# Kernel tuning notes

Measured on AMD Instinct MI355X. Metric: run time of the kernel, lower is better.

## Reference

```python
import jax, jax.numpy as jnp
import numpy as np

N_IN = 100000
N_OUT = 100000
K = 27        # kernel_volume = 3^3 for 3D hypercube kernel
M = 50000     # matched (in,out) pairs per kernel offset
C_IN = 128
C_OUT = 128


def setup_inputs() -> dict:
    key = jax.random.key(0)
    k1, k2, k3, k4, k5 = jax.random.split(key, 5)
    features = jax.random.normal(k1, (N_IN, C_IN), dtype=jnp.float32)
    kernel = jax.random.normal(k2, (K, C_IN, C_OUT), dtype=jnp.float32) * (1.0 / np.sqrt(C_IN * K))
    bias = jax.random.normal(k3, (1, C_OUT), dtype=jnp.float32) * 0.01
    in_map = jax.random.randint(k4, (K, M), 0, N_IN, dtype=jnp.int32)
    out_map = jax.random.randint(k5, (K, M), 0, N_OUT, dtype=jnp.int32)
    return {"features": features, "kernel": kernel, "bias": bias,
            "in_map": in_map, "out_map": out_map, "n_out": N_OUT}


def reference(features, kernel, bias, in_map, out_map, n_out):
    # Sparse convolution: per-offset gather -> GEMM -> scatter-add.
    gathered = features[in_map]                          # [K, M, C_in]
    prod = jnp.einsum('kmc,kcd->kmd', gathered, kernel)  # [K, M, C_out]
    out = jnp.zeros((n_out, kernel.shape[-1]), dtype=features.dtype)
    out = out.at[out_map.reshape(-1)].add(prod.reshape(-1, kernel.shape[-1]))
    out = out + bias                                     # bias broadcast [1, C_out]
    return out
```

## Files before the change

kernel.cpp:

```cpp
#include <hip/hip_runtime.h>
#include <hip/hip_bf16.h>

typedef __attribute__((ext_vector_type(4))) float  f32x4;
typedef __attribute__((ext_vector_type(8))) short  bf16x8;
typedef __attribute__((ext_vector_type(2))) float  float2v;
typedef __attribute__((ext_vector_type(4))) float  float4v;
typedef __attribute__((ext_vector_type(8))) unsigned short ushort8;
typedef __attribute__((ext_vector_type(2))) unsigned int uint2v;

#define CIO 128
#define BR  64
#define MAXT 96
#define NB_MAX 2048
#define CSPLIT 8
#define NPASS 6
#define STAGE_CAP 14336

__device__ __forceinline__ unsigned short f2bf(float f) {
  unsigned int u = __float_as_uint(f);
  u = u + 0x7fffu + ((u >> 16) & 1u);
  return (unsigned short)(u >> 16);
}
__device__ __forceinline__ float bf2f(unsigned short u) {
  return __uint_as_float(((unsigned int)u) << 16);
}

__device__ __forceinline__ void wgbar() {
  asm volatile("s_waitcnt lgkmcnt(0)" ::: "memory");
  __builtin_amdgcn_s_barrier();
  __builtin_amdgcn_sched_barrier(0);
}

__global__ void prep_wswz(const float* __restrict__ W,
                          unsigned short* __restrict__ Wswz, int total) {
  int i = blockIdx.x * 256 + threadIdx.x;
  if (i >= total) return;
  int lane = i & 63;
  int nf   = (i >> 6) & 7;
  int kb   = (i >> 9) & 3;
  int k    = i >> 11;
  int n    = nf * 16 + (lane & 15);
  int c0   = kb * 32 + (lane >> 4) * 8;
  ushort8 v;
  #pragma unroll
  for (int e = 0; e < 8; ++e)
    v[e] = f2bf(W[k * 16384 + (c0 + e) * 128 + n]);
  *(ushort8*)(Wswz + (size_t)i * 8) = v;
}

__global__ void prep_fbf(const float* __restrict__ f,
                         unsigned short* __restrict__ fbf, int total8) {
  int i = blockIdx.x * 256 + threadIdx.x;
  if (i >= total8) return;
  const float4v* s = (const float4v*)(f + (size_t)i * 8);
  float4v v0 = s[0], v1 = s[1];
  ushort8 o;
  o[0] = f2bf(v0.x); o[1] = f2bf(v0.y); o[2] = f2bf(v0.z); o[3] = f2bf(v0.w);
  o[4] = f2bf(v1.x); o[5] = f2bf(v1.y); o[6] = f2bf(v1.z); o[7] = f2bf(v1.w);
  *(ushort8*)(fbf + (size_t)i * 8) = o;
}

__global__ __launch_bounds__(1024) void count27p(const int* __restrict__ out_map,
                                                 int* __restrict__ counts,
                                                 int M, int NB, int nkey) {
  __shared__ int h[NB_MAX];
  int k = blockIdx.x, s = blockIdx.y, t = threadIdx.x;
  for (int i = t; i < NB; i += 1024) h[i] = 0;
  __syncthreads();
  int m0 = (int)(((long)s * M) / CSPLIT), m1 = (int)(((long)(s + 1) * M) / CSPLIT);
  for (int m = m0 + t; m < m1; m += 1024)
    atomicAdd(&h[out_map[k * M + m] / BR], 1);
  __syncthreads();
  for (int i = t; i < NB; i += 1024)
    counts[s * nkey + k * NB + i] = h[i];
}

__global__ __launch_bounds__(1024) void scan_p1(const int* __restrict__ counts,
                                                int* __restrict__ offs,
                                                int* __restrict__ bsum, int nkey) {
  __shared__ int part[1024];
  const int t = threadIdx.x;
  const int i = blockIdx.x * 1024 + t;
  int v = 0;
  if (i < nkey) {
    #pragma unroll
    for (int sl = 0; sl < CSPLIT; ++sl) v += counts[sl * nkey + i];
  }
  part[t] = v;
  __syncthreads();
  for (int d = 1; d < 1024; d <<= 1) {
    int x = (t >= d) ? part[t - d] : 0;
    __syncthreads();
    part[t] += x;
    __syncthreads();
  }
  if (i < nkey) offs[i] = part[t] - v;
  if (t == 1023) bsum[blockIdx.x] = part[1023];
}
__global__ void scan_p2(int* __restrict__ bsum, int nb) {
  if (threadIdx.x == 0) {
    int run = 0;
    for (int i = 0; i < nb; ++i) { int c = bsum[i]; bsum[i] = run; run += c; }
    bsum[nb] = run;
  }
}
__global__ __launch_bounds__(1024) void scan_p3(int* __restrict__ offs,
                                                const int* __restrict__ bsum,
                                                int nkey, int nb) {
  const int i = blockIdx.x * 1024 + threadIdx.x;
  if (i < nkey) offs[i] += bsum[blockIdx.x];
  if (i == 0) offs[nkey] = bsum[nb];
}

__global__ __launch_bounds__(1024) void scatter27c(const int* __restrict__ in_map,
                                                   const int* __restrict__ out_map,
                                                   const int* __restrict__ offs,
                                                   unsigned int* __restrict__ sorted,
                                                   int M, int NB) {
  __shared__ unsigned int stage[STAGE_CAP];
  __shared__ int pos[384];
  const int k = blockIdx.x, p = blockIdx.y, t = threadIdx.x;
  const int b0 = (int)(((long)p * NB) / NPASS);
  const int b1 = (int)(((long)(p + 1) * NB) / NPASS);
  const int nb = b1 - b0;
  const int sbase = offs[k * NB + b0];
  const int send  = offs[k * NB + b1];
  const int size  = send - sbase;
  for (int i = t; i < nb; i += 1024) pos[i] = offs[k * NB + b0 + i] - sbase;
  __syncthreads();
  if (size <= STAGE_CAP) {
    for (int m = t; m < M; m += 1024) {
      int o = out_map[k * M + m];
      int bkt = o / BR;
      if (bkt >= b0 && bkt < b1) {
        int q = atomicAdd(&pos[bkt - b0], 1);
        stage[q] = ((unsigned int)in_map[k * M + m] << 7) | (unsigned int)(o & (BR - 1));
      }
    }
    __syncthreads();
    for (int i = t; i < size; i += 1024) sorted[sbase + i] = stage[i];
  } else {
    for (int m = t; m < M; m += 1024) {
      int o = out_map[k * M + m];
      int bkt = o / BR;
      if (bkt >= b0 && bkt < b1) {
        int q = atomicAdd(&pos[bkt - b0], 1);
        sorted[sbase + q] = ((unsigned int)in_map[k * M + m] << 7) | (unsigned int)(o & (BR - 1));
      }
    }
  }
}

__device__ __forceinline__ void load_w(const unsigned int* __restrict__ sorted,
                                       const int* tb, const int* te,
                                       int T, int ntiles, int l16,
                                       unsigned int& w0, unsigned int& w1) {
  w0 = 64u; w1 = 64u;
  if (T < ntiles) {
    int base = tb[T], e = te[T];
    int i0 = base + l16, i1 = base + 16 + l16;
    if (i0 < e) w0 = sorted[i0];
    if (i1 < e) w1 = sorted[i1];
  }
}
__device__ __forceinline__ void load_a(const unsigned short* __restrict__ fbf,
                                       unsigned int w0, unsigned int w1, int lk,
                                       bf16x8* a0, bf16x8* a1) {
  int in0 = (int)(w0 >> 7), in1 = (int)(w1 >> 7);
  #pragma unroll
  for (int kb = 0; kb < 4; ++kb) {
    a0[kb] = *(const bf16x8*)(fbf + (size_t)in0 * CIO + kb * 32 + lk * 8);
    a1[kb] = *(const bf16x8*)(fbf + (size_t)in1 * CIO + kb * 32 + lk * 8);
  }
}
__device__ __forceinline__ void compute_tile(const unsigned short* __restrict__ wk,
                                             const bf16x8 a0[4], const bf16x8 a1[4],
                                             unsigned char* smem,
                                             int wave, int lane, int l16, int lk, int swz) {
  #pragma unroll
  for (int h = 0; h < 2; ++h) {
    f32x4 acc[2][4] = {};
    #pragma unroll
    for (int kb = 0; kb < 4; ++kb) {
      const unsigned short* wkb = wk + kb * 4096 + h * 2048;
      #pragma unroll
      for (int nf = 0; nf < 4; ++nf) {
        bf16x8 bfr = *(const bf16x8*)(wkb + nf * 512 + lane * 8);
        acc[0][nf] = __builtin_amdgcn_mfma_f32_16x16x32_bf16(a0[kb], bfr, acc[0][nf], 0, 0, 0);
        acc[1][nf] = __builtin_amdgcn_mfma_f32_16x16x32_bf16(a1[kb], bfr, acc[1][nf], 0, 0, 0);
      }
    }
    #pragma unroll
    for (int rg = 0; rg < 2; ++rg)
      #pragma unroll
      for (int nf = 0; nf < 4; ++nf) {
        unsigned int lo = f2bf(acc[rg][nf][0]) | ((unsigned int)f2bf(acc[rg][nf][1]) << 16);
        unsigned int hi = f2bf(acc[rg][nf][2]) | ((unsigned int)f2bf(acc[rg][nf][3]) << 16);
        int c  = h * 64 + nf * 16 + l16;
        int eb = (wave * 32 + rg * 16 + lk * 4) * 2;
        *(uint2v*)&smem[c * 256 + (eb ^ swz)] = (uint2v){lo, hi};
      }
  }
}
__device__ __forceinline__ void reduce_cs(const unsigned char* __restrict__ lrow,
                                          const unsigned char* __restrict__ smem,
                                          f32x4 racc[4][2],
                                          int cb, int l16, int lk, int swz) {
  #pragma unroll
  for (int kb = 0; kb < 4; ++kb) {
    unsigned long long lr8 = *(const unsigned long long*)&lrow[kb * 32 + lk * 8];
    int eb[8];
    #pragma unroll
    for (int j = 0; j < 8; ++j) eb[j] = (int)((lr8 >> (8 * j)) & 255ull);
    const int eoff = ((kb * 32 + lk * 8) * 2) ^ swz;
    bf16x8 bq0 = *(const bf16x8*)&smem[(cb + l16) * 256 + eoff];
    bf16x8 bq1 = *(const bf16x8*)&smem[(cb + 16 + l16) * 256 + eoff];
    #pragma unroll
    for (int mt = 0; mt < 4; ++mt) {
      const int target = mt * 16 + l16;
      union { unsigned int u[4]; bf16x8 v; } su;
      #pragma unroll
      for (int p = 0; p < 4; ++p)
        su.u[p] = (eb[2 * p] == target ? 0x3F80u : 0u) |
                  (eb[2 * p + 1] == target ? 0x3F800000u : 0u);
      racc[mt][0] = __builtin_amdgcn_mfma_f32_16x16x32_bf16(su.v, bq0, racc[mt][0], 0, 0, 0);
      racc[mt][1] = __builtin_amdgcn_mfma_f32_16x16x32_bf16(su.v, bq1, racc[mt][1], 0, 0, 0);
    }
  }
}

__global__ __launch_bounds__(256) void spconv_fused(
    const unsigned short* __restrict__ fbf,
    const unsigned short* __restrict__ Wswz,
    const unsigned int* __restrict__ sorted,
    const int* __restrict__ offs,
    const float* __restrict__ bias,
    float* __restrict__ out,
    int NB, int n_out, int KVOL) {
  __shared__ __align__(16) unsigned char smem[32768];
  __shared__ __align__(8)  unsigned char lrow_lds[2][128];
  __shared__ unsigned char tile_k[MAXT];
  __shared__ int tile_base[MAXT], tile_end[MAXT];
  __shared__ int seg_s[32], seg_c[32];
  __shared__ int ntiles_sh;

  const int b    = blockIdx.x;
  const int tid  = threadIdx.x;
  const int wave = tid >> 6;
  const int lane = tid & 63;
  const int l16  = lane & 15;
  const int lk   = lane >> 4;
  const int swz  = (l16 & 7) << 4;
  const int cb   = wave * 32;

  if (tid < KVOL) {
    int s = offs[tid * NB + b], e = offs[tid * NB + b + 1];
    seg_s[tid] = s; seg_c[tid] = e - s;
  }
  __syncthreads();
  if (tid == 0) {
    int nt = 0;
    for (int k = 0; k < KVOL; ++k) {
      int s = seg_s[k], c = seg_c[k];
      for (int t = 0; t < c; t += 32)
        if (nt < MAXT) { tile_k[nt] = (unsigned char)k; tile_base[nt] = s + t; tile_end[nt] = s + c; ++nt; }
    }
    ntiles_sh = nt;
  }
  f32x4 racc[4][2];
  #pragma unroll
  for (int i = 0; i < 4; ++i) {
    racc[i][0] = (f32x4){0.f, 0.f, 0.f, 0.f};
    racc[i][1] = (f32x4){0.f, 0.f, 0.f, 0.f};
  }
  __syncthreads();
  const int ntiles = ntiles_sh;
  const int nbatch = (ntiles + 3) >> 2;

  unsigned int wA0, wA1, wB0, wB1;
  bf16x8 aA0[4], aA1[4], aB0[4], aB1[4];
  load_w(sorted, tile_base, tile_end, wave, ntiles, l16, wA0, wA1);
  if (lk == 0) {
    lrow_lds[0][wave * 32 + l16]      = (unsigned char)(wA0 & 127u);
    lrow_lds[0][wave * 32 + 16 + l16] = (unsigned char)(wA1 & 127u);
  }
  load_a(fbf, wA0, wA1, lk, aA0, aA1);
  load_w(sorted, tile_base, tile_end, 4 + wave, ntiles, l16, wB0, wB1);

  for (int bt = 0; bt < nbatch; bt += 2) {
    {
      const int T = bt * 4 + wave;
      if (T < ntiles)
        compute_tile(Wswz + (size_t)tile_k[T] * 16384, aA0, aA1, smem, wave, lane, l16, lk, swz);
      wgbar();
      load_a(fbf, wB0, wB1, lk, aB0, aB1);
      load_w(sorted, tile_base, tile_end, (bt + 2) * 4 + wave, ntiles, l16, wA0, wA1);
      reduce_cs(lrow_lds[0], smem, racc, cb, l16, lk, swz);
      wgbar();
      if (lk == 0) {
        lrow_lds[1][wave * 32 + l16]      = (unsigned char)(wB0 & 127u);
        lrow_lds[1][wave * 32 + 16 + l16] = (unsigned char)(wB1 & 127u);
      }
    }
    {
      const int T = (bt + 1) * 4 + wave;
      if (T < ntiles)
        compute_tile(Wswz + (size_t)tile_k[T] * 16384, aB0, aB1, smem, wave, lane, l16, lk, swz);
      wgbar();
      load_a(fbf, wA0, wA1, lk, aA0, aA1);
      load_w(sorted, tile_base, tile_end, (bt + 3) * 4 + wave, ntiles, l16, wB0, wB1);
      reduce_cs(lrow_lds[1], smem, racc, cb, l16, lk, swz);
      wgbar();
      if (lk == 0) {
        lrow_lds[0][wave * 32 + l16]      = (unsigned char)(wA0 & 127u);
        lrow_lds[0][wave * 32 + 16 + l16] = (unsigned char)(wA1 & 127u);
      }
    }
  }

  {
    const float bi0 = bias[cb + l16];
    const float bi1 = bias[cb + 16 + l16];
    #pragma unroll
    for (int mt = 0; mt < 4; ++mt)
      #pragma unroll
      for (int r = 0; r < 4; ++r) {
        int orow = b * BR + mt * 16 + lk * 4 + r;
        if (orow < n_out) {
          out[(size_t)orow * CIO + cb + l16]      = racc[mt][0][r] + bi0;
          out[(size_t)orow * CIO + cb + 16 + l16] = racc[mt][1][r] + bi1;
        }
      }
  }
}

__global__ void prep_weights(const float* __restrict__ W,
                             unsigned short* __restrict__ Wt, int total) {
  int idx = blockIdx.x * 256 + threadIdx.x;
  if (idx >= total) return;
  int k  = idx >> 14;
  int n  = (idx >> 7) & 127;
  int kk = idx & 127;
  Wt[idx] = f2bf(W[k * 16384 + kk * 128 + n]);
}
__global__ void init_bias(float* __restrict__ out,
                          const float* __restrict__ bias, int total4) {
  int idx = blockIdx.x * 256 + threadIdx.x;
  if (idx >= total4) return;
  float4v b = ((const float4v*)bias)[idx & 31];
  ((float4v*)out)[idx] = b;
}
__global__ __launch_bounds__(256) void spconv_mfma_legacy(
    const float* __restrict__ features, const unsigned short* __restrict__ Wt,
    const int* __restrict__ in_map, const int* __restrict__ out_map,
    float* __restrict__ out, int M) {
  const int ky = blockIdx.y, m0 = blockIdx.x * 64, tid = threadIdx.x;
  __shared__ unsigned short Alds[64 * CIO];
  __shared__ unsigned short Blds[CIO * CIO];
  {
    const ushort8* src = (const ushort8*)(Wt + ky * 16384);
    #pragma unroll
    for (int i = 0; i < 8; ++i) {
      int chunk = tid + i * 256, byte = chunk * 16;
      int row = byte >> 8, off = byte & 255, sw = off ^ ((row & 7) << 4);
      *(ushort8*)((char*)Blds + row * 256 + sw) = src[chunk];
    }
  }
  {
    int r = tid >> 2, q = tid & 3, m = m0 + r;
    unsigned short tmp[32];
    if (m < M) {
      int frow = in_map[ky * M + m];
      const float4v* src = (const float4v*)(features + frow * CIO + q * 32);
      #pragma unroll
      for (int i = 0; i < 8; ++i) {
        float4v v = src[i];
        tmp[i*4+0]=f2bf(v.x); tmp[i*4+1]=f2bf(v.y); tmp[i*4+2]=f2bf(v.z); tmp[i*4+3]=f2bf(v.w);
      }
    } else {
      #pragma unroll
      for (int i = 0; i < 32; ++i) tmp[i] = 0;
    }
    #pragma unroll
    for (int c = 0; c < 4; ++c) {
      int off = q * 64 + c * 16, sw = off ^ ((r & 7) << 4);
      *(ushort8*)((char*)Alds + r * 256 + sw) = *(ushort8*)(tmp + c * 8);
    }
  }
  __syncthreads();
  const int wid = tid >> 6, lane = tid & 63;
  const int wm = wid >> 1, wn = wid & 1, l16 = lane & 15, lk = lane >> 4;
  f32x4 acc[2][4] = {};
  #pragma unroll
  for (int kb = 0; kb < CIO; kb += 32) {
    bf16x8 af[2], bfr[4];
    #pragma unroll
    for (int mf = 0; mf < 2; ++mf) {
      int row = wm * 32 + mf * 16 + l16, off = (kb + lk * 8) * 2;
      int sw = off ^ ((row & 7) << 4);
      af[mf] = *(const bf16x8*)((const char*)Alds + row * 256 + sw);
    }
    #pragma unroll
    for (int nf = 0; nf < 4; ++nf) {
      int n = wn * 64 + nf * 16 + l16, off = (kb + lk * 8) * 2;
      int sw = off ^ ((n & 7) << 4);
      bfr[nf] = *(const bf16x8*)((const char*)Blds + n * 256 + sw);
    }
    #pragma unroll
    for (int mf = 0; mf < 2; ++mf)
      #pragma unroll
      for (int nf = 0; nf < 4; ++nf)
        acc[mf][nf] = __builtin_amdgcn_mfma_f32_16x16x32_bf16(af[mf], bfr[nf], acc[mf][nf], 0, 0, 0);
  }
  #pragma unroll
  for (int mf = 0; mf < 2; ++mf)
    #pragma unroll
    for (int r = 0; r < 4; ++r) {
      int mrow = wm * 32 + mf * 16 + lk * 4 + r, m = m0 + mrow;
      if (m < M) {
        int orow = out_map[ky * M + m];
        float* dst = out + orow * CIO + wn * 64 + l16;
        #pragma unroll
        for (int nf = 0; nf < 4; ++nf) unsafeAtomicAdd(dst + nf * 16, acc[mf][nf][r]);
      }
    }
}

static inline size_t align256(size_t x) { return (x + 255) & ~(size_t)255; }

extern "C" void kernel_launch(void* const* d_in, const int* in_sizes, int n_in,
                              void* d_out, int out_size, void* d_ws, size_t ws_size,
                              hipStream_t stream) {
  const float* features = (const float*)d_in[0];
  const float* W        = (const float*)d_in[1];
  const float* bias     = (const float*)d_in[2];
  const int*   in_map   = (const int*)d_in[3];
  const int*   out_map  = (const int*)d_in[4];
  float*       out      = (float*)d_out;

  const int KVOL  = in_sizes[1] / (CIO * CIO);
  const int M     = in_sizes[3] / KVOL;
  const int n_out = out_size / CIO;
  const int N_IN  = in_sizes[0] / CIO;
  const int NB    = (n_out + BR - 1) / BR;
  const int NKEY  = KVOL * NB;
  const size_t KM = (size_t)KVOL * M;

  const size_t s_wswz = (size_t)KVOL * CIO * CIO * 2;
  const size_t o_cnt  = align256(s_wswz);
  const size_t o_offs = align256(o_cnt + (size_t)CSPLIT * NKEY * 4);
  const size_t o_bsum = align256(o_offs + ((size_t)NKEY + 1) * 4);
  const size_t o_sort = align256(o_bsum + 4096 * 4);
  const size_t o_fbf  = align256(o_sort + KM * 4);
  const size_t need   = o_fbf + (size_t)N_IN * CIO * 2;

  if (NB <= NB_MAX && KVOL <= 32 && ws_size >= need) {
    unsigned short* Wswz   = (unsigned short*)d_ws;
    int*            cnt    = (int*)((char*)d_ws + o_cnt);
    int*            offs   = (int*)((char*)d_ws + o_offs);
    int*            bsum   = (int*)((char*)d_ws + o_bsum);
    unsigned int*   sorted = (unsigned int*)((char*)d_ws + o_sort);
    unsigned short* fbf    = (unsigned short*)((char*)d_ws + o_fbf);

    int wtot = KVOL * 4 * 8 * 64;
    prep_wswz<<<(wtot + 255) / 256, 256, 0, stream>>>(W, Wswz, wtot);
    int total8 = N_IN * CIO / 8;
    prep_fbf<<<(total8 + 255) / 256, 256, 0, stream>>>(features, fbf, total8);
    count27p<<<dim3(KVOL, CSPLIT), 1024, 0, stream>>>(out_map, cnt, M, NB, NKEY);

    const int nsb = (NKEY + 1023) / 1024;
    scan_p1<<<nsb, 1024, 0, stream>>>(cnt, offs, bsum, NKEY);
    scan_p2<<<1, 64, 0, stream>>>(bsum, nsb);
    scan_p3<<<nsb, 1024, 0, stream>>>(offs, bsum, NKEY, nsb);

    scatter27c<<<dim3(KVOL, NPASS), 1024, 0, stream>>>(in_map, out_map, offs, sorted, M, NB);

    spconv_fused<<<NB, 256, 0, stream>>>(fbf, Wswz, sorted, offs, bias, out,
                                         NB, n_out, KVOL);
  } else {
    unsigned short* Wt = (unsigned short*)d_ws;
    if (ws_size < s_wswz) return;
    int wtot = KVOL * CIO * CIO;
    prep_weights<<<(wtot + 255) / 256, 256, 0, stream>>>(W, Wt, wtot);
    int total4 = out_size / 4;
    init_bias<<<(total4 + 255) / 256, 256, 0, stream>>>(out, bias, total4);
    dim3 grid((M + 63) / 64, KVOL);
    spconv_mfma_legacy<<<grid, 256, 0, stream>>>(features, Wt, in_map, out_map, out, M);
  }
}
```

Before: 340.9 us.

## Assign one output bucket per wave instead of per workgroup, dropping block barriers

```diff
diff --git a/kernel.cpp b/kernel.cpp
--- a/kernel.cpp
+++ b/kernel.cpp
@@ -3,14 +3,13 @@
 
 typedef __attribute__((ext_vector_type(4))) float  f32x4;
 typedef __attribute__((ext_vector_type(8))) short  bf16x8;
-typedef __attribute__((ext_vector_type(2))) float  float2v;
 typedef __attribute__((ext_vector_type(4))) float  float4v;
 typedef __attribute__((ext_vector_type(8))) unsigned short ushort8;
 typedef __attribute__((ext_vector_type(2))) unsigned int uint2v;
 
 #define CIO 128
 #define BR  64
-#define MAXT 96
+#define MAXTW 80
 #define NB_MAX 2048
 #define CSPLIT 8
 #define NPASS 6
@@ -21,13 +20,9 @@
   u = u + 0x7fffu + ((u >> 16) & 1u);
   return (unsigned short)(u >> 16);
 }
-__device__ __forceinline__ float bf2f(unsigned short u) {
-  return __uint_as_float(((unsigned int)u) << 16);
-}
-
-__device__ __forceinline__ void wgbar() {
+
+__device__ __forceinline__ void wave_fence() {
   asm volatile("s_waitcnt lgkmcnt(0)" ::: "memory");
-  __builtin_amdgcn_s_barrier();
   __builtin_amdgcn_sched_barrier(0);
 }
 
@@ -173,10 +168,10 @@
     a1[kb] = *(const bf16x8*)(fbf + (size_t)in1 * CIO + kb * 32 + lk * 8);
   }
 }
-__device__ __forceinline__ void compute_tile(const unsigned short* __restrict__ wk,
-                                             const bf16x8 a0[4], const bf16x8 a1[4],
-                                             unsigned char* smem,
-                                             int wave, int lane, int l16, int lk, int swz) {
+__device__ __forceinline__ void compute_tile_w(const unsigned short* __restrict__ wk,
+                                               const bf16x8 a0[4], const bf16x8 a1[4],
+                                               unsigned char* sg,
+                                               int lane, int l16, int lk, int swz) {
   #pragma unroll
   for (int h = 0; h < 2; ++h) {
     f32x4 acc[2][4] = {};
@@ -197,39 +192,39 @@
         unsigned int lo = f2bf(acc[rg][nf][0]) | ((unsigned int)f2bf(acc[rg][nf][1]) << 16);
         unsigned int hi = f2bf(acc[rg][nf][2]) | ((unsigned int)f2bf(acc[rg][nf][3]) << 16);
         int c  = h * 64 + nf * 16 + l16;
-        int eb = (wave * 32 + rg * 16 + lk * 4) * 2;
-        *(uint2v*)&smem[c * 256 + (eb ^ swz)] = (uint2v){lo, hi};
-      }
-  }
-}
-__device__ __forceinline__ void reduce_cs(const unsigned char* __restrict__ lrow,
-                                          const unsigned char* __restrict__ smem,
-                                          f32x4 racc[4][2],
-                                          int cb, int l16, int lk, int swz) {
-  #pragma unroll
-  for (int kb = 0; kb < 4; ++kb) {
-    unsigned long long lr8 = *(const unsigned long long*)&lrow[kb * 32 + lk * 8];
-    int eb[8];
-    #pragma unroll
-    for (int j = 0; j < 8; ++j) eb[j] = (int)((lr8 >> (8 * j)) & 255ull);
-    const int eoff = ((kb * 32 + lk * 8) * 2) ^ swz;
-    bf16x8 bq0 = *(const bf16x8*)&smem[(cb + l16) * 256 + eoff];
-    bf16x8 bq1 = *(const bf16x8*)&smem[(cb + 16 + l16) * 256 + eoff];
-    #pragma unroll
-    for (int mt = 0; mt < 4; ++mt) {
-      const int target = mt * 16 + l16;
-      union { unsigned int u[4]; bf16x8 v; } su;
-      #pragma unroll
-      for (int p = 0; p < 4; ++p)
-        su.u[p] = (eb[2 * p] == target ? 0x3F80u : 0u) |
-                  (eb[2 * p + 1] == target ? 0x3F800000u : 0u);
-      racc[mt][0] = __builtin_amdgcn_mfma_f32_16x16x32_bf16(su.v, bq0, racc[mt][0], 0, 0, 0);
-      racc[mt][1] = __builtin_amdgcn_mfma_f32_16x16x32_bf16(su.v, bq1, racc[mt][1], 0, 0, 0);
-    }
-  }
-}
-
-__global__ __launch_bounds__(256) void spconv_fused(
+        int eb = (rg * 16 + lk * 4) * 2;
+        *(uint2v*)&sg[c * 128 + (eb ^ swz)] = (uint2v){lo, hi};
+      }
+  }
+}
+__device__ __forceinline__ void reduce_w(const unsigned char* __restrict__ lrow,
+                                         const unsigned char* __restrict__ sg,
+                                         f32x4 racc[4][8],
+                                         int l16, int lk, int swz) {
+  unsigned long long lr8 = *(const unsigned long long*)&lrow[lk * 8];
+  int eb8[8];
+  #pragma unroll
+  for (int j = 0; j < 8; ++j) eb8[j] = (int)((lr8 >> (8 * j)) & 255ull);
+  union { unsigned int u[4]; bf16x8 v; } su[4];
+  #pragma unroll
+  for (int mt = 0; mt < 4; ++mt) {
+    const int target = mt * 16 + l16;
+    #pragma unroll
+    for (int p = 0; p < 4; ++p)
+      su[mt].u[p] = (eb8[2 * p] == target ? 0x3F80u : 0u) |
+                    (eb8[2 * p + 1] == target ? 0x3F800000u : 0u);
+  }
+  const int eoff = (lk * 16) ^ swz;
+  #pragma unroll
+  for (int nf = 0; nf < 8; ++nf) {
+    bf16x8 bq = *(const bf16x8*)&sg[(nf * 16 + l16) * 128 + eoff];
+    #pragma unroll
+    for (int mt = 0; mt < 4; ++mt)
+      racc[mt][nf] = __builtin_amdgcn_mfma_f32_16x16x32_bf16(su[mt].v, bq, racc[mt][nf], 0, 0, 0);
+  }
+}
+
+__global__ __launch_bounds__(256) void spconv_wave(
     const unsigned short* __restrict__ fbf,
     const unsigned short* __restrict__ Wswz,
     const unsigned int* __restrict__ sorted,
@@ -237,98 +232,89 @@
     const float* __restrict__ bias,
     float* __restrict__ out,
     int NB, int n_out, int KVOL) {
-  __shared__ __align__(16) unsigned char smem[32768];
-  __shared__ __align__(8)  unsigned char lrow_lds[2][128];
-  __shared__ unsigned char tile_k[MAXT];
-  __shared__ int tile_base[MAXT], tile_end[MAXT];
-  __shared__ int seg_s[32], seg_c[32];
-  __shared__ int ntiles_sh;
-
-  const int b    = blockIdx.x;
-  const int tid  = threadIdx.x;
-  const int wave = tid >> 6;
-  const int lane = tid & 63;
+  __shared__ __align__(16) unsigned char stag[4][16384];
+  __shared__ __align__(8)  unsigned char lrowb[4][2][32];
+  __shared__ int tb[4][MAXTW], te[4][MAXTW];
+  __shared__ unsigned char tkk[4][MAXTW];
+
+  const int wave = threadIdx.x >> 6;
+  const int lane = threadIdx.x & 63;
   const int l16  = lane & 15;
   const int lk   = lane >> 4;
   const int swz  = (l16 & 7) << 4;
-  const int cb   = wave * 32;
-
-  if (tid < KVOL) {
-    int s = offs[tid * NB + b], e = offs[tid * NB + b + 1];
-    seg_s[tid] = s; seg_c[tid] = e - s;
-  }
-  __syncthreads();
-  if (tid == 0) {
-    int nt = 0;
-    for (int k = 0; k < KVOL; ++k) {
-      int s = seg_s[k], c = seg_c[k];
+  const int bucket = blockIdx.x * 4 + wave;
+  if (bucket >= NB) return;
+
+  int vs = 0, vc = 0;
+  if (lane < KVOL) {
+    vs = offs[lane * NB + bucket];
+    vc = offs[lane * NB + bucket + 1] - vs;
+  }
+  int ntr = 0;
+  for (int k = 0; k < KVOL; ++k) {
+    int s = __shfl(vs, k), c = __shfl(vc, k);
+    if (lane == 0) {
       for (int t = 0; t < c; t += 32)
-        if (nt < MAXT) { tile_k[nt] = (unsigned char)k; tile_base[nt] = s + t; tile_end[nt] = s + c; ++nt; }
-    }
-    ntiles_sh = nt;
-  }
-  f32x4 racc[4][2];
-  #pragma unroll
-  for (int i = 0; i < 4; ++i) {
-    racc[i][0] = (f32x4){0.f, 0.f, 0.f, 0.f};
-    racc[i][1] = (f32x4){0.f, 0.f, 0.f, 0.f};
-  }
-  __syncthreads();
-  const int ntiles = ntiles_sh;
-  const int nbatch = (ntiles + 3) >> 2;
+        if (ntr < MAXTW) { tkk[wave][ntr] = (unsigned char)k; tb[wave][ntr] = s + t; te[wave][ntr] = s + c; ++ntr; }
+    }
+  }
+  const int nt = __shfl(ntr, 0);
+  wave_fence();
+
+  f32x4 racc[4][8];
+  #pragma unroll
+  for (int mt = 0; mt < 4; ++mt)
+    #pragma unroll
+    for (int nf = 0; nf < 8; ++nf) racc[mt][nf] = (f32x4){0.f, 0.f, 0.f, 0.f};
 
   unsigned int wA0, wA1, wB0, wB1;
   bf16x8 aA0[4], aA1[4], aB0[4], aB1[4];
-  load_w(sorted, tile_base, tile_end, wave, ntiles, l16, wA0, wA1);
+  load_w(sorted, tb[wave], te[wave], 0, nt, l16, wA0, wA1);
   if (lk == 0) {
-    lrow_lds[0][wave * 32 + l16]      = (unsigned char)(wA0 & 127u);
-    lrow_lds[0][wave * 32 + 16 + l16] = (unsigned char)(wA1 & 127u);
+    lrowb[wave][0][l16]      = (unsigned char)(wA0 & 127u);
+    lrowb[wave][0][16 + l16] = (unsigned char)(wA1 & 127u);
   }
   load_a(fbf, wA0, wA1, lk, aA0, aA1);
-  load_w(sorted, tile_base, tile_end, 4 + wave, ntiles, l16, wB0, wB1);
-
-  for (int bt = 0; bt < nbatch; bt += 2) {
-    {
-      const int T = bt * 4 + wave;
-      if (T < ntiles)
-        compute_tile(Wswz + (size_t)tile_k[T] * 16384, aA0, aA1, smem, wave, lane, l16, lk, swz);
-      wgbar();
-      load_a(fbf, wB0, wB1, lk, aB0, aB1);
-      load_w(sorted, tile_base, tile_end, (bt + 2) * 4 + wave, ntiles, l16, wA0, wA1);
-      reduce_cs(lrow_lds[0], smem, racc, cb, l16, lk, swz);
-      wgbar();
-      if (lk == 0) {
-        lrow_lds[1][wave * 32 + l16]      = (unsigned char)(wB0 & 127u);
-        lrow_lds[1][wave * 32 + 16 + l16] = (unsigned char)(wB1 & 127u);
-      }
-    }
-    {
-      const int T = (bt + 1) * 4 + wave;
-      if (T < ntiles)
-        compute_tile(Wswz + (size_t)tile_k[T] * 16384, aB0, aB1, smem, wave, lane, l16, lk, swz);
-      wgbar();
-      load_a(fbf, wA0, wA1, lk, aA0, aA1);
-      load_w(sorted, tile_base, tile_end, (bt + 3) * 4 + wave, ntiles, l16, wB0, wB1);
-      reduce_cs(lrow_lds[1], smem, racc, cb, l16, lk, swz);
-      wgbar();
-      if (lk == 0) {
-        lrow_lds[0][wave * 32 + l16]      = (unsigned char)(wA0 & 127u);
-        lrow_lds[0][wave * 32 + 16 + l16] = (unsigned char)(wA1 & 127u);
-      }
-    }
+  load_w(sorted, tb[wave], te[wave], 1, nt, l16, wB0, wB1);
+
+  for (int bt = 0; bt < nt; bt += 2) {
+    wave_fence();
+    compute_tile_w(Wswz + (size_t)tkk[wave][bt] * 16384, aA0, aA1, stag[wave], lane, l16, lk, swz);
+    load_a(fbf, wB0, wB1, lk, aB0, aB1);
+    load_w(sorted, tb[wave], te[wave], bt + 2, nt, l16, wA0, wA1);
+    if (lk == 0) {
+      lrowb[wave][1][l16]      = (unsigned char)(wB0 & 127u);
+      lrowb[wave][1][16 + l16] = (unsigned char)(wB1 & 127u);
+    }
+    wave_fence();
+    reduce_w(&lrowb[wave][0][0], stag[wave], racc, l16, lk, swz);
+
+    wave_fence();
+    if (bt + 1 < nt)
+      compute_tile_w(Wswz + (size_t)tkk[wave][bt + 1] * 16384, aB0, aB1, stag[wave], lane, l16, lk, swz);
+    load_a(fbf, wA0, wA1, lk, aA0, aA1);
+    load_w(sorted, tb[wave], te[wave], bt + 3, nt, l16, wB0, wB1);
+    if (lk == 0) {
+      lrowb[wave][0][l16]      = (unsigned char)(wA0 & 127u);
+      lrowb[wave][0][16 + l16] = (unsigned char)(wA1 & 127u);
+    }
+    wave_fence();
+    reduce_w(&lrowb[wave][1][0], stag[wave], racc, l16, lk, swz);
   }
 
   {
-    const float bi0 = bias[cb + l16];
-    const float bi1 = bias[cb + 16 + l16];
+    float bi[8];
+    #pragma unroll
+    for (int nf = 0; nf < 8; ++nf) bi[nf] = bias[nf * 16 + l16];
     #pragma unroll
     for (int mt = 0; mt < 4; ++mt)
       #pragma unroll
       for (int r = 0; r < 4; ++r) {
-        int orow = b * BR + mt * 16 + lk * 4 + r;
+        int orow = bucket * BR + mt * 16 + lk * 4 + r;
         if (orow < n_out) {
-          out[(size_t)orow * CIO + cb + l16]      = racc[mt][0][r] + bi0;
-          out[(size_t)orow * CIO + cb + 16 + l16] = racc[mt][1][r] + bi1;
+          #pragma unroll
+          for (int nf = 0; nf < 8; ++nf)
+            out[(size_t)orow * CIO + nf * 16 + l16] = racc[mt][nf][r] + bi[nf];
         }
       }
   }
@@ -475,8 +461,9 @@
 
     scatter27c<<<dim3(KVOL, NPASS), 1024, 0, stream>>>(in_map, out_map, offs, sorted, M, NB);
 
-    spconv_fused<<<NB, 256, 0, stream>>>(fbf, Wswz, sorted, offs, bias, out,
-                                         NB, n_out, KVOL);
+    const int blocksW = (NB + 3) / 4;
+    spconv_wave<<<blocksW, 256, 0, stream>>>(fbf, Wswz, sorted, offs, bias, out,
+                                             NB, n_out, KVOL);
   } else {
     unsigned short* Wt = (unsigned short*)d_ws;
     if (ws_size < s_wswz) return;
```

Result: faster. 303.0 us (-11.1%).
